# Kernel optimization log

Hardware: AMD Instinct MI355X
Metric: run time of the kernel (lower is better)

The kernel has to match this reference:

```python
import jax, jax.numpy as jnp
import numpy as np

DIM = 768
NUM_HEADS = 12
HEAD_DIM = DIM // NUM_HEADS
SCALE = HEAD_DIM ** -0.5


def setup_inputs() -> dict:
    key = jax.random.key(0)
    k1, k2, k3, k4, k5 = jax.random.split(key, 5)
    B, N, C = 4, 2048, DIM
    x = jax.random.normal(k1, (B, N, C), dtype=jnp.float32)
    xpos = jax.random.randint(k2, (B, N), 0, 2048, dtype=jnp.int32)
    # torch Linear weights: qkv (no bias), proj (with bias)
    lim_qkv = (1.0 / C) ** 0.5
    w_qkv = jax.random.uniform(k3, (3 * C, C), minval=-lim_qkv, maxval=lim_qkv, dtype=jnp.float32)
    w_proj = jax.random.uniform(k4, (C, C), minval=-lim_qkv, maxval=lim_qkv, dtype=jnp.float32)
    b_proj = jax.random.uniform(k5, (C,), minval=-lim_qkv, maxval=lim_qkv, dtype=jnp.float32)
    return {"x": x, "xpos": xpos, "w_qkv": w_qkv, "w_proj": w_proj, "b_proj": b_proj}


def reference(x, xpos, w_qkv, w_proj, b_proj):
    B, N, C = x.shape
    H, Dh = NUM_HEADS, HEAD_DIM
    # fused QKV projection: [B,N,3C] -> [B,N,3,H,Dh] -> [B,H,3,N,Dh]
    qkv = (x @ w_qkv.T).reshape(B, N, 3, H, Dh).transpose(0, 3, 2, 1, 4)
    q, k, v = qkv[:, :, 0], qkv[:, :, 1], qkv[:, :, 2]
    # rope is None -> xpos unused
    # naive attention: materialize full [B,H,N,N] scores (matches pytorch_naive)
    scores = jnp.einsum('bhqd,bhkd->bhqk', q, k) * SCALE
    attn = jax.nn.softmax(scores, axis=-1)
    out = jnp.einsum('bhqk,bhkd->bhqd', attn, v)  # [B,H,N,Dh]
    out = out.transpose(0, 2, 1, 3).reshape(B, N, C)
    return out @ w_proj.T + b_proj
```

## Files before the change

### kernel.cpp

```cpp
#include <hip/hip_runtime.h>
#include <math.h>

typedef __bf16 bf16;
typedef __attribute__((ext_vector_type(4))) __bf16 bf16x4;
typedef __attribute__((ext_vector_type(8))) __bf16 bf16x8;
typedef __attribute__((ext_vector_type(4))) float f32x4;
typedef __attribute__((ext_vector_type(4))) unsigned int u32x4;

#define AS1 __attribute__((address_space(1)))
#define AS3 __attribute__((address_space(3)))

__device__ __forceinline__ void gload16(const void* g, void* l) {
  __builtin_amdgcn_global_load_lds((const AS1 void*)g, (AS3 void*)l, 16, 0, 0);
}

__device__ __forceinline__ unsigned int pack2bf(float lo, float hi) {
  union { unsigned int u; __bf16 h[2]; } w;
  w.h[0] = (bf16)lo; w.h[1] = (bf16)hi;
  return w.u;
}

#define DIM 768
#define NH  12
#define HD  64
#define B_  4
#define N_  2048
#define M_  (B_*N_)
#define BH_ (B_*NH)

#define QSCALE 0.1803368801111244f

__global__ void convert_all(const float4* __restrict__ x,
                            const float4* __restrict__ wq,
                            const float4* __restrict__ wp,
                            bf16x4* __restrict__ xb,
                            bf16x4* __restrict__ wqb,
                            bf16x4* __restrict__ wpb) {
  const int nx = M_*DIM/4, nq = 3*DIM*DIM/4, np = DIM*DIM/4;
  const int total = nx + nq + np;
  for (int i = blockIdx.x*blockDim.x + threadIdx.x; i < total;
       i += gridDim.x*blockDim.x) {
    float4 v; bf16x4* dst;
    if (i < nx)           { v = x[i];         dst = xb  + i;         }
    else if (i < nx + nq) { v = wq[i-nx];     dst = wqb + (i-nx);    }
    else                  { v = wp[i-nx-nq];  dst = wpb + (i-nx-nq); }
    bf16x4 o = { (bf16)v.x, (bf16)v.y, (bf16)v.z, (bf16)v.w };
    *dst = o;
  }
}

template<int EPI>
__global__ __launch_bounds__(256)
void gemm_bt(const bf16* __restrict__ A, const bf16* __restrict__ B,
             bf16* __restrict__ qv, bf16* __restrict__ kv_, bf16* __restrict__ vt,
             const float* __restrict__ bprj, float* __restrict__ out) {
  constexpr int K = DIM;
  __shared__ __align__(16) bf16 As[128*32];
  __shared__ __align__(16) bf16 Bs[128*32];
  const int tid = threadIdx.x;
  const int wave = tid >> 6, lane = tid & 63;
  const int l15 = lane & 15, lg = lane >> 4;
  const int wr = wave >> 1, wc = wave & 1;
  const int m0 = blockIdx.y * 128, n0 = blockIdx.x * 128;

  f32x4 acc[4][4] = {};
  const int pbase = wave*2048 + lane*16;

  for (int kb = 0; kb < K; kb += 32) {
    __syncthreads();
#pragma unroll
    for (int i = 0; i < 2; i++) {
      int p = pbase + i*1024;
      int row = p >> 6, cb = p & 63;
      gload16((const char*)A + ((size_t)(m0+row)*K + kb)*2 + cb, (char*)As + p);
      gload16((const char*)B + ((size_t)(n0+row)*K + kb)*2 + cb, (char*)Bs + p);
    }
    __syncthreads();
    bf16x8 af[4], bfr[4];
#pragma unroll
    for (int f = 0; f < 4; f++) {
      af[f]  = *(const bf16x8*)(As + (wr*64 + f*16 + l15)*32 + lg*8);
      bfr[f] = *(const bf16x8*)(Bs + (wc*64 + f*16 + l15)*32 + lg*8);
    }
#pragma unroll
    for (int fm = 0; fm < 4; fm++)
#pragma unroll
      for (int fn = 0; fn < 4; fn++)
        acc[fm][fn] = __builtin_amdgcn_mfma_f32_16x16x32_bf16(af[fm], bfr[fn],
                                                              acc[fm][fn], 0, 0, 0);
  }

  if (EPI == 0) {
    const int c0 = n0 + wc*64;
    const int t = c0 / DIM;
    const int hcol = (c0 % DIM) >> 6;
#pragma unroll
    for (int fm = 0; fm < 4; fm++) {
      const int gm0 = m0 + wr*64 + fm*16 + (lg<<2);
      const int b = gm0 >> 11, nn0 = gm0 & 2047;
      const size_t bh = (size_t)b*NH + hcol;
#pragma unroll
      for (int fn = 0; fn < 4; fn++) {
        const int d = fn*16 + l15;
        if (t == 0) {
#pragma unroll
          for (int r = 0; r < 4; r++)
            qv[(bh*N_ + nn0 + r)*HD + d] = (bf16)(acc[fm][fn][r] * QSCALE);
        } else if (t == 1) {
#pragma unroll
          for (int r = 0; r < 4; r++)
            kv_[(bh*N_ + nn0 + r)*HD + d] = (bf16)acc[fm][fn][r];
        } else {
          bf16x4 pk = { (bf16)acc[fm][fn][0], (bf16)acc[fm][fn][1],
                        (bf16)acc[fm][fn][2], (bf16)acc[fm][fn][3] };
          *(bf16x4*)(vt + (bh*HD + d)*N_ + nn0) = pk;
        }
      }
    }
  } else {
#pragma unroll
    for (int fn = 0; fn < 4; fn++) {
      const int c = n0 + wc*64 + fn*16 + l15;
      const float bias = bprj[c];
#pragma unroll
      for (int fm = 0; fm < 4; fm++) {
        const int gm0 = m0 + wr*64 + fm*16 + (lg<<2);
#pragma unroll
        for (int r = 0; r < 4; r++)
          out[(size_t)(gm0 + r)*DIM + c] = acc[fm][fn][r] + bias;
      }
    }
  }
}

__global__ __launch_bounds__(256)
void attn_fwd(const bf16* __restrict__ Q, const bf16* __restrict__ Kb,
              const bf16* __restrict__ Vt, bf16* __restrict__ AO) {
  __shared__ __align__(16) bf16 Ks[2][64*64];
  __shared__ __align__(16) bf16 Vs[2][64*64];
  const int tid = threadIdx.x;
  const int wave = tid >> 6, lane = tid & 63;
  const int l15 = lane & 15, lg = lane >> 4;
  const int bh = blockIdx.y;
  const int b = bh / NH, h = bh % NH;
  const int q0 = blockIdx.x*64 + wave*16;

  const bf16* Qbase = Q + (size_t)bh*N_*HD;
  bf16x8 qf[2];
#pragma unroll
  for (int ks = 0; ks < 2; ks++)
    qf[ks] = *(const bf16x8*)(Qbase + (size_t)(q0 + l15)*HD + ks*32 + lg*8);

  f32x4 Ot[4] = {};
  float m_ = -INFINITY, l_ = 0.f;

  const char* Kg = (const char*)(Kb + (size_t)bh*N_*HD);
  const char* Vg = (const char*)(Vt + (size_t)bh*HD*N_);
  const int pbase = wave*2048 + lane*16;
  const bool lower = (lane < 32);
  const bool q03 = (lg == 0) || (lg == 3);

#define STAGE(buf, kv)                                                      \
  {                                                                         \
    _Pragma("unroll")                                                       \
    for (int i = 0; i < 2; i++) {                                           \
      int p = pbase + i*1024;                                               \
      int r = p >> 7, cbp = p & 127;                                        \
      int cb = cbp ^ ((r & 7) << 4);                                        \
      gload16(Kg + (size_t)((kv) + r)*128 + cb, (char*)Ks[buf] + p);        \
      gload16(Vg + (size_t)r*(N_*2) + (kv)*2 + cb, (char*)Vs[buf] + p);     \
    }                                                                       \
  }

  STAGE(0, 0);

  for (int t = 0; t < N_/64; ++t) {
    __syncthreads();
    if (t + 1 < N_/64) STAGE((t+1)&1, (t+1)*64);
    const char* Kc = (const char*)Ks[t&1];
    const char* Vc = (const char*)Vs[t&1];

    f32x4 s[4] = {};
#pragma unroll
    for (int ks = 0; ks < 2; ks++) {
      bf16x8 kf[4];
#pragma unroll
      for (int fk = 0; fk < 4; fk++) {
        int r = fk*16 + l15;
        int cb = (ks*64 + lg*16) ^ ((r & 7) << 4);
        kf[fk] = *(const bf16x8*)(Kc + r*128 + cb);
      }
#pragma unroll
      for (int fk = 0; fk < 4; fk++)
        s[fk] = __builtin_amdgcn_mfma_f32_16x16x32_bf16(kf[fk], qf[ks],
                                                        s[fk], 0, 0, 0);
    }

    f32x4 m01, m23, m4;
#pragma unroll
    for (int r = 0; r < 4; r++) {
      m01[r] = fmaxf(s[0][r], s[1][r]);
      m23[r] = fmaxf(s[2][r], s[3][r]);
      m4[r]  = fmaxf(m01[r], m23[r]);
    }
    float mx = fmaxf(fmaxf(m4[0], m4[1]), fmaxf(m4[2], m4[3]));
    mx = fmaxf(mx, __shfl_xor(mx, 16));
    mx = fmaxf(mx, __shfl_xor(mx, 32));
    if (!__all(mx - m_ <= 8.0f)) {
      float mn = fmaxf(m_, mx);
      float c = exp2f(m_ - mn);
      m_ = mn; l_ *= c;
#pragma unroll
      for (int fd = 0; fd < 4; fd++) Ot[fd] *= c;
    }
    float pe[4][4]; float rs = 0.f;
#pragma unroll
    for (int fk = 0; fk < 4; fk++)
#pragma unroll
      for (int r = 0; r < 4; r++) {
        pe[fk][r] = exp2f(s[fk][r] - m_);
        rs += pe[fk][r];
      }
    rs += __shfl_xor(rs, 16);
    rs += __shfl_xor(rs, 32);
    l_ += rs;

    unsigned int pk[4][2];
#pragma unroll
    for (int fk = 0; fk < 4; fk++)
#pragma unroll
      for (int rp = 0; rp < 2; rp++)
        pk[fk][rp] = pack2bf(pe[fk][2*rp], pe[fk][2*rp+1]);

    unsigned int Eo[2][2], Er[2][2], rB[2][2];
#pragma unroll
    for (int fh = 0; fh < 2; fh++)
#pragma unroll
      for (int rp = 0; rp < 2; rp++) {
        unsigned int vA = lower ? pk[2*fh+1][rp] : pk[2*fh][rp];
        Er[fh][rp] = __shfl_xor((int)vA, 32);
        Eo[fh][rp] = lower ? pk[2*fh][rp] : pk[2*fh+1][rp];
      }
#pragma unroll
    for (int fh = 0; fh < 2; fh++)
#pragma unroll
      for (int rp = 0; rp < 2; rp++) {
        unsigned int vB = q03 ? Er[fh][rp] : Eo[fh][rp];
        rB[fh][rp] = __shfl_xor((int)vB, 16);
      }
    unsigned int paw[2][4];
#pragma unroll
    for (int ks = 0; ks < 2; ks++)
#pragma unroll
      for (int rp = 0; rp < 2; rp++) {
        paw[ks][rp]   = (lg == 0) ? Eo[ks][rp] :
                        (lg == 1) ? rB[ks][rp] :
                        (lg == 2) ? Er[ks][rp] : rB[ks][rp];
        paw[ks][2+rp] = (lg == 0) ? rB[ks][rp] :
                        (lg == 1) ? Er[ks][rp] :
                        (lg == 2) ? rB[ks][rp] : Eo[ks][rp];
      }

#pragma unroll
    for (int ks = 0; ks < 2; ks++) {
      bf16x8 vb[4];
#pragma unroll
      for (int fd = 0; fd < 4; fd++) {
        int r = fd*16 + l15;
        int cb = (ks*64 + lg*16) ^ ((r & 7) << 4);
        vb[fd] = *(const bf16x8*)(Vc + r*128 + cb);
      }
      u32x4 tw = { paw[ks][0], paw[ks][1], paw[ks][2], paw[ks][3] };
      bf16x8 pa = __builtin_bit_cast(bf16x8, tw);
#pragma unroll
      for (int fd = 0; fd < 4; fd++)
        Ot[fd] = __builtin_amdgcn_mfma_f32_16x16x32_bf16(vb[fd], pa,
                                                         Ot[fd], 0, 0, 0);
    }
  }

  const float inv = 1.f / l_;
  const int qrow = q0 + l15;
#pragma unroll
  for (int fd = 0; fd < 4; fd++) {
    bf16x4 pk4 = { (bf16)(Ot[fd][0]*inv), (bf16)(Ot[fd][1]*inv),
                   (bf16)(Ot[fd][2]*inv), (bf16)(Ot[fd][3]*inv) };
    *(bf16x4*)(AO + ((size_t)b*N_ + qrow)*DIM + h*HD + fd*16 + lg*4) = pk4;
  }
#undef STAGE
}

extern "C" void kernel_launch(void* const* d_in, const int* in_sizes, int n_in,
                              void* d_out, int out_size, void* d_ws, size_t ws_size,
                              hipStream_t stream) {
  const float* x     = (const float*)d_in[0];
  const float* wqkv  = (const float*)d_in[2];
  const float* wproj = (const float*)d_in[3];
  const float* bproj = (const float*)d_in[4];
  float* out = (float*)d_out;

  char* ws = (char*)d_ws;
  bf16* xb    = (bf16*)ws;  ws += (size_t)M_*DIM*2;
  bf16* wqkvb = (bf16*)ws;  ws += (size_t)3*DIM*DIM*2;
  bf16* wprojb= (bf16*)ws;  ws += (size_t)DIM*DIM*2;
  bf16* qb    = (bf16*)ws;  ws += (size_t)BH_*N_*HD*2;
  bf16* kb    = (bf16*)ws;  ws += (size_t)BH_*N_*HD*2;
  bf16* vtb   = (bf16*)ws;  ws += (size_t)BH_*HD*N_*2;
  bf16* aob   = (bf16*)ws;  ws += (size_t)M_*DIM*2;

  convert_all<<<dim3(2048), dim3(256), 0, stream>>>(
      (const float4*)x, (const float4*)wqkv, (const float4*)wproj,
      (bf16x4*)xb, (bf16x4*)wqkvb, (bf16x4*)wprojb);

  gemm_bt<0><<<dim3(3*DIM/128, M_/128), dim3(256), 0, stream>>>(
      xb, wqkvb, qb, kb, vtb, nullptr, nullptr);

  attn_fwd<<<dim3(N_/64, BH_), dim3(256), 0, stream>>>(qb, kb, vtb, aob);

  gemm_bt<1><<<dim3(DIM/128, M_/128), dim3(256), 0, stream>>>(
      aob, wprojb, nullptr, nullptr, nullptr, bproj, out);
}
```

Measured before the change: 294.6 us.

## Switch attention to 32x32x16 MFMA with 32 queries per wave

Rewrites the attention inner loop to use 32x32x16 bf16 MFMA tiles, so each wave handles 32 query rows instead of 16 and each block covers 128 queries. The P-to-A-operand repacking becomes a single cross-half shuffle instead of a multi-stage shuffle and select network. Each K/V tile loaded into LDS is reused across twice as many queries, halving K/V staging traffic per query. In exchange the grid has half as many blocks (fewer for occupancy across CUs) and each wave holds more accumulator registers.

```diff
diff --git a/kernel.cpp b/kernel.cpp
--- a/kernel.cpp
+++ b/kernel.cpp
@@ -5,6 +5,7 @@
 typedef __attribute__((ext_vector_type(4))) __bf16 bf16x4;
 typedef __attribute__((ext_vector_type(8))) __bf16 bf16x8;
 typedef __attribute__((ext_vector_type(4))) float f32x4;
+typedef __attribute__((ext_vector_type(16))) float f32x16;
 typedef __attribute__((ext_vector_type(4))) unsigned int u32x4;
 
 #define AS1 __attribute__((address_space(1)))
@@ -140,25 +141,23 @@
   __shared__ __align__(16) bf16 Vs[2][64*64];
   const int tid = threadIdx.x;
   const int wave = tid >> 6, lane = tid & 63;
-  const int l15 = lane & 15, lg = lane >> 4;
+  const int l31 = lane & 31, h = lane >> 5;
   const int bh = blockIdx.y;
-  const int b = bh / NH, h = bh % NH;
-  const int q0 = blockIdx.x*64 + wave*16;
-
-  const bf16* Qbase = Q + (size_t)bh*N_*HD;
-  bf16x8 qf[2];
-#pragma unroll
-  for (int ks = 0; ks < 2; ks++)
-    qf[ks] = *(const bf16x8*)(Qbase + (size_t)(q0 + l15)*HD + ks*32 + lg*8);
-
-  f32x4 Ot[4] = {};
+  const int b = bh / NH, hed = bh % NH;
+  const int q0 = blockIdx.x*128 + wave*32;
+
+  const bf16* Qbase = Q + ((size_t)bh*N_ + q0 + l31)*HD;
+  bf16x8 qf[4];
+#pragma unroll
+  for (int dk = 0; dk < 4; dk++)
+    qf[dk] = *(const bf16x8*)(Qbase + dk*16 + h*8);
+
+  f32x16 Ot[2] = {};
   float m_ = -INFINITY, l_ = 0.f;
 
   const char* Kg = (const char*)(Kb + (size_t)bh*N_*HD);
   const char* Vg = (const char*)(Vt + (size_t)bh*HD*N_);
   const int pbase = wave*2048 + lane*16;
-  const bool lower = (lane < 32);
-  const bool q03 = (lg == 0) || (lg == 3);
 
 #define STAGE(buf, kv)                                                      \
   {                                                                         \
@@ -180,113 +179,87 @@
     const char* Kc = (const char*)Ks[t&1];
     const char* Vc = (const char*)Vs[t&1];
 
-    f32x4 s[4] = {};
-#pragma unroll
-    for (int ks = 0; ks < 2; ks++) {
-      bf16x8 kf[4];
-#pragma unroll
-      for (int fk = 0; fk < 4; fk++) {
-        int r = fk*16 + l15;
-        int cb = (ks*64 + lg*16) ^ ((r & 7) << 4);
-        kf[fk] = *(const bf16x8*)(Kc + r*128 + cb);
-      }
-#pragma unroll
-      for (int fk = 0; fk < 4; fk++)
-        s[fk] = __builtin_amdgcn_mfma_f32_16x16x32_bf16(kf[fk], qf[ks],
-                                                        s[fk], 0, 0, 0);
-    }
-
-    f32x4 m01, m23, m4;
-#pragma unroll
-    for (int r = 0; r < 4; r++) {
-      m01[r] = fmaxf(s[0][r], s[1][r]);
-      m23[r] = fmaxf(s[2][r], s[3][r]);
-      m4[r]  = fmaxf(m01[r], m23[r]);
-    }
-    float mx = fmaxf(fmaxf(m4[0], m4[1]), fmaxf(m4[2], m4[3]));
-    mx = fmaxf(mx, __shfl_xor(mx, 16));
+    f32x16 s[2] = {};
+#pragma unroll
+    for (int kkt = 0; kkt < 2; kkt++) {
+      const int r = kkt*32 + l31;
+      const int sw = (r & 7) << 4;
+#pragma unroll
+      for (int dk = 0; dk < 4; dk++) {
+        bf16x8 kf = *(const bf16x8*)(Kc + r*128 + ((dk*32 + h*16) ^ sw));
+        s[kkt] = __builtin_amdgcn_mfma_f32_32x32x16_bf16(kf, qf[dk],
+                                                         s[kkt], 0, 0, 0);
+      }
+    }
+
+    float mx = s[0][0];
+#pragma unroll
+    for (int i = 1; i < 16; i++) mx = fmaxf(mx, s[0][i]);
+#pragma unroll
+    for (int i = 0; i < 16; i++) mx = fmaxf(mx, s[1][i]);
     mx = fmaxf(mx, __shfl_xor(mx, 32));
     if (!__all(mx - m_ <= 8.0f)) {
       float mn = fmaxf(m_, mx);
       float c = exp2f(m_ - mn);
       m_ = mn; l_ *= c;
 #pragma unroll
-      for (int fd = 0; fd < 4; fd++) Ot[fd] *= c;
-    }
-    float pe[4][4]; float rs = 0.f;
-#pragma unroll
-    for (int fk = 0; fk < 4; fk++)
-#pragma unroll
-      for (int r = 0; r < 4; r++) {
-        pe[fk][r] = exp2f(s[fk][r] - m_);
-        rs += pe[fk][r];
-      }
-    rs += __shfl_xor(rs, 16);
+      for (int dt = 0; dt < 2; dt++)
+#pragma unroll
+        for (int i = 0; i < 16; i++) Ot[dt][i] *= c;
+    }
+    float rs = 0.f;
+#pragma unroll
+    for (int kkt = 0; kkt < 2; kkt++)
+#pragma unroll
+      for (int i = 0; i < 16; i++) {
+        float p = exp2f(s[kkt][i] - m_);
+        s[kkt][i] = p;
+        rs += p;
+      }
     rs += __shfl_xor(rs, 32);
     l_ += rs;
 
-    unsigned int pk[4][2];
-#pragma unroll
-    for (int fk = 0; fk < 4; fk++)
-#pragma unroll
-      for (int rp = 0; rp < 2; rp++)
-        pk[fk][rp] = pack2bf(pe[fk][2*rp], pe[fk][2*rp+1]);
-
-    unsigned int Eo[2][2], Er[2][2], rB[2][2];
-#pragma unroll
-    for (int fh = 0; fh < 2; fh++)
-#pragma unroll
-      for (int rp = 0; rp < 2; rp++) {
-        unsigned int vA = lower ? pk[2*fh+1][rp] : pk[2*fh][rp];
-        Er[fh][rp] = __shfl_xor((int)vA, 32);
-        Eo[fh][rp] = lower ? pk[2*fh][rp] : pk[2*fh+1][rp];
-      }
-#pragma unroll
-    for (int fh = 0; fh < 2; fh++)
-#pragma unroll
-      for (int rp = 0; rp < 2; rp++) {
-        unsigned int vB = q03 ? Er[fh][rp] : Eo[fh][rp];
-        rB[fh][rp] = __shfl_xor((int)vB, 16);
-      }
-    unsigned int paw[2][4];
-#pragma unroll
-    for (int ks = 0; ks < 2; ks++)
-#pragma unroll
-      for (int rp = 0; rp < 2; rp++) {
-        paw[ks][rp]   = (lg == 0) ? Eo[ks][rp] :
-                        (lg == 1) ? rB[ks][rp] :
-                        (lg == 2) ? Er[ks][rp] : rB[ks][rp];
-        paw[ks][2+rp] = (lg == 0) ? rB[ks][rp] :
-                        (lg == 1) ? Er[ks][rp] :
-                        (lg == 2) ? rB[ks][rp] : Eo[ks][rp];
-      }
-
-#pragma unroll
-    for (int ks = 0; ks < 2; ks++) {
-      bf16x8 vb[4];
-#pragma unroll
-      for (int fd = 0; fd < 4; fd++) {
-        int r = fd*16 + l15;
-        int cb = (ks*64 + lg*16) ^ ((r & 7) << 4);
-        vb[fd] = *(const bf16x8*)(Vc + r*128 + cb);
-      }
-      u32x4 tw = { paw[ks][0], paw[ks][1], paw[ks][2], paw[ks][3] };
-      bf16x8 pa = __builtin_bit_cast(bf16x8, tw);
-#pragma unroll
-      for (int fd = 0; fd < 4; fd++)
-        Ot[fd] = __builtin_amdgcn_mfma_f32_16x16x32_bf16(vb[fd], pa,
-                                                         Ot[fd], 0, 0, 0);
+    unsigned int pw[4][4];
+#pragma unroll
+    for (int st = 0; st < 4; st++) {
+      const int kkt = st >> 1, base = (st & 1) * 8;
+      unsigned int a0 = pack2bf(s[kkt][base+0], s[kkt][base+1]);
+      unsigned int a1 = pack2bf(s[kkt][base+2], s[kkt][base+3]);
+      unsigned int b0 = pack2bf(s[kkt][base+4], s[kkt][base+5]);
+      unsigned int b1 = pack2bf(s[kkt][base+6], s[kkt][base+7]);
+      unsigned int r0 = __shfl_xor((int)(h ? a0 : b0), 32);
+      unsigned int r1 = __shfl_xor((int)(h ? a1 : b1), 32);
+      pw[st][0] = h ? r0 : a0;
+      pw[st][1] = h ? r1 : a1;
+      pw[st][2] = h ? b0 : r0;
+      pw[st][3] = h ? b1 : r1;
+    }
+
+#pragma unroll
+    for (int dt = 0; dt < 2; dt++) {
+      const int r = dt*32 + l31;
+      const int sw = (r & 7) << 4;
+#pragma unroll
+      for (int st = 0; st < 4; st++) {
+        bf16x8 vf = *(const bf16x8*)(Vc + r*128 + ((st*32 + h*16) ^ sw));
+        u32x4 tw = { pw[st][0], pw[st][1], pw[st][2], pw[st][3] };
+        bf16x8 pa = __builtin_bit_cast(bf16x8, tw);
+        Ot[dt] = __builtin_amdgcn_mfma_f32_32x32x16_bf16(vf, pa,
+                                                         Ot[dt], 0, 0, 0);
+      }
     }
   }
 
   const float inv = 1.f / l_;
-  const int qrow = q0 + l15;
-#pragma unroll
-  for (int fd = 0; fd < 4; fd++) {
-    bf16x4 pk4 = { (bf16)(Ot[fd][0]*inv), (bf16)(Ot[fd][1]*inv),
-                   (bf16)(Ot[fd][2]*inv), (bf16)(Ot[fd][3]*inv) };
-    *(bf16x4*)(AO + ((size_t)b*N_ + qrow)*DIM + h*HD + fd*16 + lg*4) = pk4;
-  }
+  bf16* aoBase = AO + ((size_t)b*N_ + q0 + l31)*DIM + hed*HD;
+#pragma unroll
+  for (int dt = 0; dt < 2; dt++)
+#pragma unroll
+    for (int g = 0; g < 4; g++) {
+      bf16x4 o4 = { (bf16)(Ot[dt][4*g+0]*inv), (bf16)(Ot[dt][4*g+1]*inv),
+                    (bf16)(Ot[dt][4*g+2]*inv), (bf16)(Ot[dt][4*g+3]*inv) };
+      *(bf16x4*)(aoBase + dt*32 + 8*g + 4*h) = o4;
+    }
 #undef STAGE
 }
 
@@ -315,7 +288,7 @@
   gemm_bt<0><<<dim3(3*DIM/128, M_/128), dim3(256), 0, stream>>>(
       xb, wqkvb, qb, kb, vtb, nullptr, nullptr);
 
-  attn_fwd<<<dim3(N_/64, BH_), dim3(256), 0, stream>>>(qb, kb, vtb, aob);
+  attn_fwd<<<dim3(N_/128, BH_), dim3(256), 0, stream>>>(qb, kb, vtb, aob);
 
   gemm_bt<1><<<dim3(DIM/128, M_/128), dim3(256), 0, stream>>>(
       aob, wprojb, nullptr, nullptr, nullptr, bproj, out);
```

Result: faster. 287.6 us (-2.4%).
